# Kernel tuning notes

Measured on AMD Instinct MI355X. Metric: run time of the kernel, lower is better.

The kernel has to match this reference:

```python
import jax, jax.numpy as jnp
import numpy as np

N_HEAD = 16
N_KV_HEAD = 4
HEAD_DIM = 128
EPS = 1e-6


def apply_rotary_emb(x, cos, sin):
    # x: (B,T,H,hd); cos/sin: (1,T,1,hd//2)
    d = x.shape[3] // 2
    x1, x2 = x[..., :d], x[..., d:]
    y1 = x1 * cos + x2 * sin
    y2 = x1 * -sin + x2 * cos
    return jnp.concatenate([y1, y2], axis=3).astype(x.dtype)


def rmsnorm(x):
    # flax nnx.RMSNorm with use_scale=False: x * rsqrt(mean(x^2) + eps)
    ms = jnp.mean(jnp.square(x), axis=-1, keepdims=True)
    return (x * jax.lax.rsqrt(ms + EPS)).astype(x.dtype)


def setup_inputs() -> dict:
    key = jax.random.key(0)
    ks = jax.random.split(key, 7)
    B, T, C = 4, 2048, 2048
    s = 0.02
    return {
        "x": jax.random.normal(ks[0], (B, T, C), jnp.float32),
        "cos": jax.random.normal(ks[1], (1, T, 1, HEAD_DIM // 2), jnp.float32),
        "sin": jax.random.normal(ks[2], (1, T, 1, HEAD_DIM // 2), jnp.float32),
        "Wq": jax.random.normal(ks[3], (C, N_HEAD * HEAD_DIM), jnp.float32) * s,
        "Wk": jax.random.normal(ks[4], (C, N_KV_HEAD * HEAD_DIM), jnp.float32) * s,
        "Wv": jax.random.normal(ks[5], (C, N_KV_HEAD * HEAD_DIM), jnp.float32) * s,
        "Wo": jax.random.normal(ks[6], (C, C), jnp.float32) * s,
    }


def reference(x, cos, sin, Wq, Wk, Wv, Wo):
    B, T, C = x.shape
    q = (x @ Wq).reshape(B, T, N_HEAD, HEAD_DIM)
    k = (x @ Wk).reshape(B, T, N_KV_HEAD, HEAD_DIM)
    v = (x @ Wv).reshape(B, T, N_KV_HEAD, HEAD_DIM)
    q = rmsnorm(apply_rotary_emb(q, cos, sin))
    k = rmsnorm(apply_rotary_emb(k, cos, sin))
    # (B,H,T,hd)
    q = jnp.transpose(q, (0, 2, 1, 3))
    k = jnp.transpose(k, (0, 2, 1, 3))
    v = jnp.transpose(v, (0, 2, 1, 3))
    nrep = N_HEAD // N_KV_HEAD
    k = jnp.repeat(k, nrep, axis=1)
    v = jnp.repeat(v, nrep, axis=1)
    scale = 1.0 / jnp.sqrt(jnp.float32(HEAD_DIM))
    att = jnp.einsum('bhqd,bhkd->bhqk', q, k) * scale
    mask = jnp.tril(jnp.ones((T, T), dtype=bool))[None, None, :, :]
    att = jnp.where(mask, att, -jnp.inf)
    att = jax.nn.softmax(att, axis=-1)
    y = jnp.einsum('bhqk,bhkd->bhqd', att, v)
    y = jnp.transpose(y, (0, 2, 1, 3)).reshape(B, T, -1)
    return y @ Wo
```

## Files before the change

### kernel.cpp

```cpp
#include <hip/hip_runtime.h>
#include <hip/hip_bf16.h>

typedef __attribute__((ext_vector_type(8))) short short8;
typedef __attribute__((ext_vector_type(4))) float f32x4;

#define B_SZ 4
#define T_SEQ 2048
#define C_DIM 2048
#define NH 16
#define NKV 4
#define HD 128

__device__ __forceinline__ unsigned short f2bf(float f) {
  union { __hip_bfloat16 h; unsigned short u; } v;
  v.h = __float2bfloat16(f);
  return v.u;
}
__device__ __forceinline__ float bf2f(unsigned short u) {
  union { unsigned short u; __hip_bfloat16 h; } v;
  v.u = u;
  return __bfloat162float(v.h);
}

__device__ __forceinline__ void gload_lds16(const unsigned short* g, unsigned short* l) {
  __builtin_amdgcn_global_load_lds(
      (const __attribute__((address_space(1))) unsigned int*)g,
      (__attribute__((address_space(3))) unsigned int*)l, 16, 0, 0);
}

__global__ void cast_x(const float* __restrict__ x, unsigned short* __restrict__ xb, int n4) {
  int i = blockIdx.x * blockDim.x + threadIdx.x;
  if (i < n4) {
    float4 f = ((const float4*)x)[i];
    ushort4 u = make_ushort4(f2bf(f.x), f2bf(f.y), f2bf(f.z), f2bf(f.w));
    ((ushort4*)xb)[i] = u;
  }
}

__global__ void wtrans(const float* __restrict__ W, unsigned short* __restrict__ Wt, int K, int N) {
  __shared__ float tile[32][33];
  int k0 = blockIdx.x * 32, n0 = blockIdx.y * 32;
  int tx = threadIdx.x, ty = threadIdx.y;
#pragma unroll
  for (int i = 0; i < 4; i++)
    tile[ty + i * 8][tx] = W[(size_t)(k0 + ty + i * 8) * N + n0 + tx];
  __syncthreads();
#pragma unroll
  for (int i = 0; i < 4; i++)
    Wt[(size_t)(n0 + ty + i * 8) * K + k0 + tx] = f2bf(tile[tx][ty + i * 8]);
}

__global__ void vtrans(const unsigned short* __restrict__ qkv, unsigned short* __restrict__ Vt) {
  __shared__ unsigned short tile[32][34];
  int t0 = blockIdx.x * 32, d0 = blockIdx.y * 32;
  int b = blockIdx.z >> 2, kvh = blockIdx.z & 3;
  int tx = threadIdx.x, ty = threadIdx.y;
#pragma unroll
  for (int i = 0; i < 4; i++)
    tile[ty + i * 8][tx] =
        qkv[(size_t)(b * T_SEQ + t0 + ty + i * 8) * 3072 + 2560 + kvh * HD + d0 + tx];
  __syncthreads();
#pragma unroll
  for (int i = 0; i < 4; i++)
    Vt[((size_t)(b * NKV + kvh) * HD + d0 + ty + i * 8) * T_SEQ + t0 + tx] = tile[tx][ty + i * 8];
}

template <typename OutT>
__global__ __launch_bounds__(256, 2) void gemm_bt(const unsigned short* __restrict__ A,
                                                  const unsigned short* __restrict__ Bt,
                                                  OutT* __restrict__ Cc, int M, int N, int K) {
  __shared__ alignas(16) unsigned short lA[128 * 32];
  __shared__ alignas(16) unsigned short lB[128 * 32];
  const int tid = threadIdx.x, lane = tid & 63, wid = tid >> 6;
  const int wr = wid >> 1, wc = wid & 1;
  const size_t row0 = (size_t)blockIdx.x * 128, col0 = (size_t)blockIdx.y * 128;
  const int lr = lane >> 2, lc = (lane & 3) * 8;
  f32x4 zero = {0.f, 0.f, 0.f, 0.f};
  f32x4 acc[4][4];
#pragma unroll
  for (int m = 0; m < 4; m++)
#pragma unroll
    for (int n = 0; n < 4; n++) acc[m][n] = zero;

  for (int k0 = 0; k0 < K; k0 += 32) {
#pragma unroll
    for (int j = 0; j < 2; ++j) {
      int chunk = wid * 2 + j;
      gload_lds16(A + (row0 + chunk * 16 + lr) * K + k0 + lc, lA + chunk * 512);
      gload_lds16(Bt + (col0 + chunk * 16 + lr) * K + k0 + lc, lB + chunk * 512);
    }
    __syncthreads();
    short8 af[4], bfr[4];
#pragma unroll
    for (int m = 0; m < 4; m++)
      af[m] = *(const short8*)(lA + (wr * 64 + m * 16 + (lane & 15)) * 32 + (lane >> 4) * 8);
#pragma unroll
    for (int n = 0; n < 4; n++)
      bfr[n] = *(const short8*)(lB + (wc * 64 + n * 16 + (lane & 15)) * 32 + (lane >> 4) * 8);
#pragma unroll
    for (int m = 0; m < 4; m++)
#pragma unroll
      for (int n = 0; n < 4; n++)
        acc[m][n] = __builtin_amdgcn_mfma_f32_16x16x32_bf16(af[m], bfr[n], acc[m][n], 0, 0, 0);
    __syncthreads();
  }
#pragma unroll
  for (int m = 0; m < 4; m++) {
#pragma unroll
    for (int n = 0; n < 4; n++) {
      size_t r = row0 + wr * 64 + m * 16 + (lane >> 4) * 4;
      size_t c = col0 + wc * 64 + n * 16 + (lane & 15);
#pragma unroll
      for (int j = 0; j < 4; j++) {
        if constexpr (sizeof(OutT) == 2)
          Cc[(r + j) * N + c] = f2bf(acc[m][n][j]);
        else
          Cc[(r + j) * N + c] = acc[m][n][j];
      }
    }
  }
}

template <int NHEADS>
__global__ void ropenorm(const unsigned short* __restrict__ qkv, int colbase,
                         const float* __restrict__ cosp, const float* __restrict__ sinp,
                         unsigned short* __restrict__ qout, float outscale) {
  int gid = blockIdx.x * 4 + (threadIdx.x >> 6);
  int lane = threadIdx.x & 63;
  int h = gid % NHEADS;
  int bt = gid / NHEADS;
  int t = bt % T_SEQ, b = bt / T_SEQ;
  const unsigned short* src = qkv + (size_t)(b * T_SEQ + t) * 3072 + colbase + h * HD;
  float x1 = bf2f(src[lane]), x2 = bf2f(src[64 + lane]);
  float c = cosp[t * 64 + lane], s = sinp[t * 64 + lane];
  float y1 = x1 * c + x2 * s;
  float y2 = x2 * c - x1 * s;
  float ss = y1 * y1 + y2 * y2;
#pragma unroll
  for (int d = 1; d < 64; d <<= 1) ss += __shfl_xor(ss, d);
  float r = rsqrtf(ss * (1.f / 128.f) + 1e-6f) * outscale;
  unsigned short* dst = qout + ((size_t)(b * NHEADS + h) * T_SEQ + t) * HD;
  dst[lane] = f2bf(y1 * r);
  dst[64 + lane] = f2bf(y2 * r);
}

__device__ __forceinline__ int swzP(int row) {
  return (row & 7) ^ (((row >> 3) & 1) << 1);
}

__global__ __launch_bounds__(256, 2) void attn(const unsigned short* __restrict__ Qn,
                                               const unsigned short* __restrict__ Kn,
                                               const unsigned short* __restrict__ Vt,
                                               unsigned short* __restrict__ Y) {
  __shared__ alignas(16) unsigned short lK[2][64 * 128];
  __shared__ alignas(16) unsigned short lV[2][128 * 64];
  __shared__ alignas(16) unsigned short pl[4][32 * 64];

  int lin = blockIdx.x;
  int low3 = lin & 7, rest = lin >> 3;
  int chi = rest >> 6, idx = rest & 63;
  int c = (chi << 3) | low3;
  int b = c >> 2, kvh = c & 3;
  int h = kvh * 4 + (idx >> 4);
  int qt = 15 - (idx & 15);
  int Q0 = qt * 128;

  int lane = threadIdx.x & 63, w = threadIdx.x >> 6;
  const int r16 = lane & 15, q4 = lane >> 4;
  const unsigned short* Qp = Qn + ((size_t)(b * NH + h) * T_SEQ + Q0 + w * 32) * HD;
  const unsigned short* Kp = Kn + (size_t)(b * NKV + kvh) * T_SEQ * HD;
  const unsigned short* Vp = Vt + (size_t)(b * NKV + kvh) * HD * T_SEQ;

  short8 qf[2][4];
#pragma unroll
  for (int m = 0; m < 2; m++)
#pragma unroll
    for (int i = 0; i < 4; i++)
      qf[m][i] = *(const short8*)(Qp + (m * 16 + r16) * HD + i * 32 + q4 * 8);

  f32x4 zero = {0.f, 0.f, 0.f, 0.f};
  f32x4 o[2][8];
  float mrow[2][4], Lp[2][4];
#pragma unroll
  for (int m = 0; m < 2; m++) {
#pragma unroll
    for (int nb = 0; nb < 8; nb++) o[m][nb] = zero;
#pragma unroll
    for (int j = 0; j < 4; j++) { mrow[m][j] = -1e30f; Lp[m][j] = 0.f; }
  }

  auto stageK = [&](int kv0, int buf) {
#pragma unroll
    for (int j = 0; j < 4; ++j) {
      int cw = w * 4 + j;
      int row = cw * 4 + (lane >> 4);
      int cb = lane & 15;
      gload_lds16(Kp + (size_t)(kv0 + row) * HD + ((cb ^ (row & 7)) * 8), &lK[buf][cw * 512]);
    }
  };
  auto stageV = [&](int kv0, int buf) {
#pragma unroll
    for (int j = 0; j < 4; ++j) {
      int cw = w * 4 + j;
      int row = cw * 8 + (lane >> 3);
      int db = lane & 7;
      gload_lds16(Vp + (size_t)row * T_SEQ + kv0 + ((db ^ (row & 7)) * 8), &lV[buf][cw * 512]);
    }
  };

  const int ntiles = 2 * qt + 2;
  const int ntw = (Q0 + w * 32 + 95) >> 6;

  stageK(0, 0);
  stageV(0, 0);
  __syncthreads();
  int cur = 0;

  for (int t = 0; t < ntiles; ++t) {
    int kv0 = t * 64;
    if (t + 1 < ntiles) { stageK(kv0 + 64, cur ^ 1); stageV(kv0 + 64, cur ^ 1); }
    if (t < ntw) {
      f32x4 s[2][4];
      __builtin_amdgcn_s_setprio(1);
#pragma unroll
      for (int nt = 0; nt < 4; nt++) {
        f32x4 a0 = zero, a1 = zero;
        int krow = nt * 16 + r16;
#pragma unroll
        for (int i = 0; i < 4; i++) {
          short8 kf =
              *(const short8*)(&lK[cur][krow * 128 + ((q4 * 8 + i * 32) ^ ((krow & 7) << 3))]);
          a0 = __builtin_amdgcn_mfma_f32_16x16x32_bf16(qf[0][i], kf, a0, 0, 0, 0);
          a1 = __builtin_amdgcn_mfma_f32_16x16x32_bf16(qf[1][i], kf, a1, 0, 0, 0);
        }
        s[0][nt] = a0;
        s[1][nt] = a1;
      }
      __builtin_amdgcn_s_setprio(0);
      if (kv0 + 63 > Q0 + w * 32) {
#pragma unroll
        for (int m = 0; m < 2; m++)
#pragma unroll
          for (int nt = 0; nt < 4; nt++)
#pragma unroll
            for (int j = 0; j < 4; j++) {
              int col = kv0 + nt * 16 + r16;
              int row = Q0 + w * 32 + m * 16 + q4 * 4 + j;
              if (col > row) s[m][nt][j] = -1e30f;
            }
      }
      float pm[2][4];
#pragma unroll
      for (int m = 0; m < 2; m++)
#pragma unroll
        for (int j = 0; j < 4; j++)
          pm[m][j] = fmaxf(fmaxf(s[m][0][j], s[m][1][j]), fmaxf(s[m][2][j], s[m][3][j]));
#pragma unroll
      for (int d = 1; d < 16; d <<= 1)
#pragma unroll
        for (int m = 0; m < 2; m++)
#pragma unroll
          for (int j = 0; j < 4; j++) pm[m][j] = fmaxf(pm[m][j], __shfl_xor(pm[m][j], d));
      float dmax = -1e30f;
#pragma unroll
      for (int m = 0; m < 2; m++)
#pragma unroll
        for (int j = 0; j < 4; j++) dmax = fmaxf(dmax, pm[m][j] - mrow[m][j]);
      if (!__all(dmax <= 8.0f)) {
#pragma unroll
        for (int m = 0; m < 2; m++)
#pragma unroll
          for (int j = 0; j < 4; j++) {
            float mn = fmaxf(mrow[m][j], pm[m][j]);
            float al = __expf(mrow[m][j] - mn);
            mrow[m][j] = mn;
            Lp[m][j] *= al;
#pragma unroll
            for (int nb = 0; nb < 8; nb++) o[m][nb][j] *= al;
          }
      }
#pragma unroll
      for (int m = 0; m < 2; m++)
#pragma unroll
        for (int nt = 0; nt < 4; nt++)
#pragma unroll
          for (int j = 0; j < 4; j++) {
            float p = __expf(s[m][nt][j] - mrow[m][j]);
            Lp[m][j] += p;
            int prow = m * 16 + q4 * 4 + j;
            pl[w][prow * 64 + ((nt * 16 + r16) ^ (swzP(prow) << 3))] = f2bf(p);
          }
      __builtin_amdgcn_s_setprio(1);
#pragma unroll
      for (int ks = 0; ks < 2; ks++) {
        int t0 = ks * 32 + q4 * 8;
        int prow0 = r16, prow1 = 16 + r16;
        short8 pf0 = *(const short8*)(&pl[w][prow0 * 64 + (t0 ^ (swzP(prow0) << 3))]);
        short8 pf1 = *(const short8*)(&pl[w][prow1 * 64 + (t0 ^ (swzP(prow1) << 3))]);
#pragma unroll
        for (int nb = 0; nb < 8; nb++) {
          int vrow = nb * 16 + r16;
          short8 vf = *(const short8*)(&lV[cur][vrow * 64 + (t0 ^ ((vrow & 7) << 3))]);
          o[0][nb] = __builtin_amdgcn_mfma_f32_16x16x32_bf16(pf0, vf, o[0][nb], 0, 0, 0);
          o[1][nb] = __builtin_amdgcn_mfma_f32_16x16x32_bf16(pf1, vf, o[1][nb], 0, 0, 0);
        }
      }
      __builtin_amdgcn_s_setprio(0);
    }
    __syncthreads();
    cur ^= 1;
  }

  float linv[2][4];
#pragma unroll
  for (int m = 0; m < 2; m++)
#pragma unroll
    for (int j = 0; j < 4; j++) {
      float v = Lp[m][j];
#pragma unroll
      for (int d = 1; d < 16; d <<= 1) v += __shfl_xor(v, d);
      linv[m][j] = 1.f / v;
    }
#pragma unroll
  for (int m = 0; m < 2; m++)
#pragma unroll
    for (int nb = 0; nb < 8; nb++)
#pragma unroll
      for (int j = 0; j < 4; j++) {
        size_t row = (size_t)Q0 + w * 32 + m * 16 + q4 * 4 + j;
        Y[((size_t)(b * T_SEQ) + row) * (NH * HD) + h * HD + nb * 16 + r16] =
            f2bf(o[m][nb][j] * linv[m][j]);
      }
}

extern "C" void kernel_launch(void* const* d_in, const int* in_sizes, int n_in,
                              void* d_out, int out_size, void* d_ws, size_t ws_size,
                              hipStream_t stream) {
  const float* x = (const float*)d_in[0];
  const float* cosp = (const float*)d_in[1];
  const float* sinp = (const float*)d_in[2];
  const float* Wq = (const float*)d_in[3];
  const float* Wk = (const float*)d_in[4];
  const float* Wv = (const float*)d_in[5];
  const float* Wo = (const float*)d_in[6];
  float* out = (float*)d_out;

  char* ws = (char*)d_ws;
  size_t off = 0;
  auto alloc = [&](size_t bytes) { void* p = ws + off; off += bytes; return p; };
  const size_t BT = (size_t)B_SZ * T_SEQ;
  unsigned short* xb = (unsigned short*)alloc(BT * C_DIM * 2);
  unsigned short* WqkvT = (unsigned short*)alloc((size_t)3072 * 2048 * 2);
  unsigned short* WoT = (unsigned short*)alloc((size_t)2048 * 2048 * 2);
  unsigned short* qkv = (unsigned short*)alloc(BT * 3072 * 2);
  unsigned short* Kb = (unsigned short*)alloc(BT * 512 * 2);
  unsigned short* Vb = (unsigned short*)alloc(BT * 512 * 2);
  unsigned short* Qb = xb;
  unsigned short* Yb = qkv;

  dim3 tb(32, 8);
  cast_x<<<16384, 256, 0, stream>>>(x, xb, (int)(BT * C_DIM / 4));
  wtrans<<<dim3(64, 64), tb, 0, stream>>>(Wq, WqkvT, 2048, 2048);
  wtrans<<<dim3(64, 16), tb, 0, stream>>>(Wk, WqkvT + (size_t)2048 * 2048, 2048, 512);
  wtrans<<<dim3(64, 16), tb, 0, stream>>>(Wv, WqkvT + (size_t)2560 * 2048, 2048, 512);
  wtrans<<<dim3(64, 64), tb, 0, stream>>>(Wo, WoT, 2048, 2048);

  gemm_bt<unsigned short><<<dim3(64, 24), 256, 0, stream>>>(xb, WqkvT, qkv, 8192, 3072, 2048);

  ropenorm<NH><<<(B_SZ * T_SEQ * NH) / 4, 256, 0, stream>>>(qkv, 0, cosp, sinp, Qb,
                                                            0.08838834764831845f);
  ropenorm<NKV><<<(B_SZ * T_SEQ * NKV) / 4, 256, 0, stream>>>(qkv, 2048, cosp, sinp, Kb, 1.0f);
  vtrans<<<dim3(64, 4, 16), tb, 0, stream>>>(qkv, Vb);

  attn<<<dim3(1024), 256, 0, stream>>>(Qb, Kb, Vb, Yb);

  gemm_bt<float><<<dim3(64, 16), 256, 0, stream>>>(Yb, WoT, out, 8192, 2048, 2048);
}
```

Baseline: 442.2 us.

## Replace 128x128 GEMM with 256x256 double-buffered swizzled GEMM using XCD remap

Replaces the simple 128x128 tile GEMM, which synchronised on every k-step, with a 512-thread 256x256 tile kernel. The new kernel uses K=64 tiles double-buffered in LDS, XOR-swizzled LDS layout, interleaved global prefetch with MFMA phases, s_setprio around MFMA bursts, and an XCD-aware block remapping for L2 locality. It aims to raise arithmetic intensity and overlap loads with compute in both projection GEMMs. The trade-off is higher register and LDS use (128KB LDS per block) and fewer blocks, which could hurt occupancy and tail behavior.

```diff
diff --git a/kernel.cpp b/kernel.cpp
--- a/kernel.cpp
+++ b/kernel.cpp
@@ -10,6 +10,8 @@
 #define NH 16
 #define NKV 4
 #define HD 128
+
+#define MFMA16 __builtin_amdgcn_mfma_f32_16x16x32_bf16
 
 __device__ __forceinline__ unsigned short f2bf(float f) {
   union { __hip_bfloat16 h; unsigned short u; } v;
@@ -66,59 +68,163 @@
 }
 
 template <typename OutT>
-__global__ __launch_bounds__(256, 2) void gemm_bt(const unsigned short* __restrict__ A,
+__global__ __launch_bounds__(512, 2) void gemm256(const unsigned short* __restrict__ A,
                                                   const unsigned short* __restrict__ Bt,
-                                                  OutT* __restrict__ Cc, int M, int N, int K) {
-  __shared__ alignas(16) unsigned short lA[128 * 32];
-  __shared__ alignas(16) unsigned short lB[128 * 32];
+                                                  OutT* __restrict__ Cc, int N, int K, int GX) {
+  __shared__ alignas(16) unsigned short lds[2][4][128 * 64];
   const int tid = threadIdx.x, lane = tid & 63, wid = tid >> 6;
-  const int wr = wid >> 1, wc = wid & 1;
-  const size_t row0 = (size_t)blockIdx.x * 128, col0 = (size_t)blockIdx.y * 128;
-  const int lr = lane >> 2, lc = (lane & 3) * 8;
+  const int wave_m = wid >> 2, wave_n = wid & 3;
+  const int r16 = lane & 15, q4 = lane >> 4;
+  const int sw = r16 & 7;
+
+  int nwg = gridDim.x, orig = blockIdx.x;
+  int qq = nwg >> 3, rr = nwg & 7;
+  int xcd = orig & 7, loc = orig >> 3;
+  int wg = (xcd < rr ? xcd * (qq + 1) : rr * (qq + 1) + (xcd - rr) * qq) + loc;
+  int bx = wg % GX, by = wg / GX;
+  const size_t row0 = (size_t)bx * 256, col0 = (size_t)by * 256;
+
+  const unsigned short* Ab0 = A + row0 * K;
+  const unsigned short* Ab1 = A + (row0 + 128) * K;
+  const unsigned short* Bb0 = Bt + col0 * K;
+  const unsigned short* Bb1 = Bt + (col0 + 128) * K;
+
+  const int srow = lane >> 3, spb = lane & 7;
+  auto stage = [&](const unsigned short* base, int buf, int slot, int k0) {
+#pragma unroll
+    for (int j = 0; j < 2; ++j) {
+      int cw = j * 8 + wid;
+      int row = cw * 8 + srow;
+      gload_lds16(base + (size_t)row * K + k0 + ((spb ^ srow) * 8), &lds[buf][slot][cw * 512]);
+    }
+  };
+
+  f32x4 acc[8][4];
   f32x4 zero = {0.f, 0.f, 0.f, 0.f};
-  f32x4 acc[4][4];
-#pragma unroll
-  for (int m = 0; m < 4; m++)
+#pragma unroll
+  for (int m = 0; m < 8; m++)
 #pragma unroll
     for (int n = 0; n < 4; n++) acc[m][n] = zero;
 
-  for (int k0 = 0; k0 < K; k0 += 32) {
-#pragma unroll
-    for (int j = 0; j < 2; ++j) {
-      int chunk = wid * 2 + j;
-      gload_lds16(A + (row0 + chunk * 16 + lr) * K + k0 + lc, lA + chunk * 512);
-      gload_lds16(Bt + (col0 + chunk * 16 + lr) * K + k0 + lc, lB + chunk * 512);
-    }
-    __syncthreads();
-    short8 af[4], bfr[4];
-#pragma unroll
-    for (int m = 0; m < 4; m++)
-      af[m] = *(const short8*)(lA + (wr * 64 + m * 16 + (lane & 15)) * 32 + (lane >> 4) * 8);
-#pragma unroll
-    for (int n = 0; n < 4; n++)
-      bfr[n] = *(const short8*)(lB + (wc * 64 + n * 16 + (lane & 15)) * 32 + (lane >> 4) * 8);
-#pragma unroll
-    for (int m = 0; m < 4; m++)
-#pragma unroll
-      for (int n = 0; n < 4; n++)
-        acc[m][n] = __builtin_amdgcn_mfma_f32_16x16x32_bf16(af[m], bfr[n], acc[m][n], 0, 0, 0);
-    __syncthreads();
+  const int NT = K / 64;
+  stage(Ab0, 0, 0, 0);
+  stage(Ab1, 0, 1, 0);
+  stage(Bb0, 0, 2, 0);
+  stage(Bb1, 0, 3, 0);
+  stage(Ab0, 1, 0, 64);
+  stage(Ab1, 1, 1, 64);
+  asm volatile("s_waitcnt vmcnt(4)" ::: "memory");
+  __builtin_amdgcn_s_barrier();
+
+  short8 af[4][2], b01[2][2], b23[2][2];
+  const int bslot = 2 + (wave_n >> 1);
+  const int bro = (wave_n & 1) * 64;
+
+  int cur = 0;
+#pragma unroll 1
+  for (int t = 0; t < NT; ++t) {
+    const unsigned short* Ah = &lds[cur][wave_m][0];
+    const unsigned short* Bh = &lds[cur][bslot][0];
+    const int k1 = t * 64 + 64, k2 = t * 64 + 128;
+#pragma unroll
+    for (int mf = 0; mf < 4; mf++)
+#pragma unroll
+      for (int kk = 0; kk < 2; kk++)
+        af[mf][kk] = *(const short8*)(Ah + (mf * 16 + r16) * 64 + (((kk * 4 + q4) ^ sw) * 8));
+#pragma unroll
+    for (int nf = 0; nf < 2; nf++)
+#pragma unroll
+      for (int kk = 0; kk < 2; kk++)
+        b01[nf][kk] =
+            *(const short8*)(Bh + (bro + nf * 16 + r16) * 64 + (((kk * 4 + q4) ^ sw) * 8));
+    if (t + 1 < NT) stage(Bb0, cur ^ 1, 2, k1);
+    __builtin_amdgcn_s_barrier();
+    asm volatile("s_waitcnt lgkmcnt(0)" ::: "memory");
+    __builtin_amdgcn_s_setprio(1);
+#pragma unroll
+    for (int mf = 0; mf < 4; mf++)
+#pragma unroll
+      for (int nf = 0; nf < 2; nf++)
+#pragma unroll
+        for (int kk = 0; kk < 2; kk++)
+          acc[mf][nf] = MFMA16(af[mf][kk], b01[nf][kk], acc[mf][nf], 0, 0, 0);
+    __builtin_amdgcn_s_setprio(0);
+    __builtin_amdgcn_s_barrier();
+#pragma unroll
+    for (int nf = 0; nf < 2; nf++)
+#pragma unroll
+      for (int kk = 0; kk < 2; kk++)
+        b23[nf][kk] =
+            *(const short8*)(Bh + (bro + (nf + 2) * 16 + r16) * 64 + (((kk * 4 + q4) ^ sw) * 8));
+    if (t + 1 < NT) stage(Bb1, cur ^ 1, 3, k1);
+    __builtin_amdgcn_s_barrier();
+    asm volatile("s_waitcnt lgkmcnt(0)" ::: "memory");
+    __builtin_amdgcn_s_setprio(1);
+#pragma unroll
+    for (int mf = 0; mf < 4; mf++)
+#pragma unroll
+      for (int nf = 0; nf < 2; nf++)
+#pragma unroll
+        for (int kk = 0; kk < 2; kk++)
+          acc[mf][nf + 2] = MFMA16(af[mf][kk], b23[nf][kk], acc[mf][nf + 2], 0, 0, 0);
+    __builtin_amdgcn_s_setprio(0);
+    __builtin_amdgcn_s_barrier();
+#pragma unroll
+    for (int mf = 0; mf < 4; mf++)
+#pragma unroll
+      for (int kk = 0; kk < 2; kk++)
+        af[mf][kk] =
+            *(const short8*)(Ah + ((mf + 4) * 16 + r16) * 64 + (((kk * 4 + q4) ^ sw) * 8));
+    __builtin_amdgcn_s_barrier();
+    asm volatile("s_waitcnt lgkmcnt(0)" ::: "memory");
+    __builtin_amdgcn_s_setprio(1);
+#pragma unroll
+    for (int mf = 0; mf < 4; mf++)
+#pragma unroll
+      for (int nf = 0; nf < 2; nf++)
+#pragma unroll
+        for (int kk = 0; kk < 2; kk++)
+          acc[mf + 4][nf] = MFMA16(af[mf][kk], b01[nf][kk], acc[mf + 4][nf], 0, 0, 0);
+    __builtin_amdgcn_s_setprio(0);
+    __builtin_amdgcn_s_barrier();
+    if (t + 2 < NT) {
+      stage(Ab0, cur, 0, k2);
+      stage(Ab1, cur, 1, k2);
+    }
+    __builtin_amdgcn_s_barrier();
+    __builtin_amdgcn_s_setprio(1);
+#pragma unroll
+    for (int mf = 0; mf < 4; mf++)
+#pragma unroll
+      for (int nf = 0; nf < 2; nf++)
+#pragma unroll
+        for (int kk = 0; kk < 2; kk++)
+          acc[mf + 4][nf + 2] = MFMA16(af[mf][kk], b23[nf][kk], acc[mf + 4][nf + 2], 0, 0, 0);
+    __builtin_amdgcn_s_setprio(0);
+    if (t + 1 < NT) {
+      if (t + 2 < NT)
+        asm volatile("s_waitcnt vmcnt(4)" ::: "memory");
+      else
+        asm volatile("s_waitcnt vmcnt(0)" ::: "memory");
+    }
+    __builtin_amdgcn_s_barrier();
+    cur ^= 1;
   }
-#pragma unroll
-  for (int m = 0; m < 4; m++) {
-#pragma unroll
-    for (int n = 0; n < 4; n++) {
-      size_t r = row0 + wr * 64 + m * 16 + (lane >> 4) * 4;
-      size_t c = col0 + wc * 64 + n * 16 + (lane & 15);
-#pragma unroll
-      for (int j = 0; j < 4; j++) {
+
+#pragma unroll
+  for (int mf = 0; mf < 8; mf++)
+#pragma unroll
+    for (int nf = 0; nf < 4; nf++) {
+      size_t rbase = row0 + wave_m * 128 + mf * 16 + q4 * 4;
+      size_t cc = col0 + wave_n * 64 + nf * 16 + r16;
+#pragma unroll
+      for (int jj = 0; jj < 4; jj++) {
         if constexpr (sizeof(OutT) == 2)
-          Cc[(r + j) * N + c] = f2bf(acc[m][n][j]);
+          Cc[(rbase + jj) * (size_t)N + cc] = f2bf(acc[mf][nf][jj]);
         else
-          Cc[(r + j) * N + c] = acc[m][n][j];
-      }
-    }
-  }
+          Cc[(rbase + jj) * (size_t)N + cc] = acc[mf][nf][jj];
+      }
+    }
 }
 
 template <int NHEADS>
@@ -365,7 +471,7 @@
   wtrans<<<dim3(64, 16), tb, 0, stream>>>(Wv, WqkvT + (size_t)2560 * 2048, 2048, 512);
   wtrans<<<dim3(64, 64), tb, 0, stream>>>(Wo, WoT, 2048, 2048);
 
-  gemm_bt<unsigned short><<<dim3(64, 24), 256, 0, stream>>>(xb, WqkvT, qkv, 8192, 3072, 2048);
+  gemm256<unsigned short><<<384, 512, 0, stream>>>(xb, WqkvT, qkv, 3072, 2048, 32);
 
   ropenorm<NH><<<(B_SZ * T_SEQ * NH) / 4, 256, 0, stream>>>(qkv, 0, cosp, sinp, Qb,
                                                             0.08838834764831845f);
@@ -374,5 +480,5 @@
 
   attn<<<dim3(1024), 256, 0, stream>>>(Qb, Kb, Vb, Yb);
 
-  gemm_bt<float><<<dim3(64, 16), 256, 0, stream>>>(Yb, WoT, out, 8192, 2048, 2048);
-}
+  gemm256<float><<<256, 512, 0, stream>>>(Yb, WoT, out, 2048, 2048, 32);
+}
```

New measurement: 434.6 us. No clear change (-1.7%).
